# Kernel tuning notes

Hardware: AMD Instinct MI355X
Metric: run time of the kernel (lower is better)

Reference implementation:

```python
import jax, jax.numpy as jnp
import numpy as np
from functools import partial

B, T, N, D_IN = 64, 12, 1024, 1
H = 64            # rnn_units
E_DIM = 16        # embed_dim
K = 2             # cheb_k
HOR, OUT = 12, 1  # horizon, output_dim
KC2 = min(12, H)  # end_conv2 kernel width


def setup_inputs() -> dict:
    key = jax.random.key(0)
    ks = jax.random.split(key, 20)
    s = 0.1
    d = {}
    d["source"] = jax.random.normal(ks[0], (B, T, N, D_IN), dtype=jnp.float32)
    d["node_emb"] = jax.random.normal(ks[1], (N, E_DIM), dtype=jnp.float32)
    # per-encoder AGCRN cell hypernetwork pools (single layer: dim_in = D_IN)
    ci = D_IN + H  # concat(x, state) channel dim
    d["e1_gate_W"] = s * jax.random.normal(ks[2], (E_DIM, K, ci, 2 * H), dtype=jnp.float32)
    d["e1_gate_b"] = s * jax.random.normal(ks[3], (E_DIM, 2 * H), dtype=jnp.float32)
    d["e1_up_W"]   = s * jax.random.normal(ks[4], (E_DIM, K, ci, H), dtype=jnp.float32)
    d["e1_up_b"]   = s * jax.random.normal(ks[5], (E_DIM, H), dtype=jnp.float32)
    d["e2_gate_W"] = s * jax.random.normal(ks[6], (E_DIM, K, ci, 2 * H), dtype=jnp.float32)
    d["e2_gate_b"] = s * jax.random.normal(ks[7], (E_DIM, 2 * H), dtype=jnp.float32)
    d["e2_up_W"]   = s * jax.random.normal(ks[8], (E_DIM, K, ci, H), dtype=jnp.float32)
    d["e2_up_b"]   = s * jax.random.normal(ks[9], (E_DIM, H), dtype=jnp.float32)
    # end convs: Conv2d(1, HOR*OUT, kernel=(1, w)) -> weight [C_out, 1, 1, w]
    d["c1_W"] = s * jax.random.normal(ks[10], (HOR * OUT, 1, 1, H), dtype=jnp.float32)
    d["c1_b"] = s * jax.random.normal(ks[11], (HOR * OUT,), dtype=jnp.float32)
    d["c2_W"] = s * jax.random.normal(ks[12], (HOR * OUT, 1, 1, KC2), dtype=jnp.float32)
    d["c2_b"] = s * jax.random.normal(ks[13], (HOR * OUT,), dtype=jnp.float32)
    d["c3_W"] = s * jax.random.normal(ks[14], (HOR * OUT, 1, 1, H), dtype=jnp.float32)
    d["c3_b"] = s * jax.random.normal(ks[15], (HOR * OUT,), dtype=jnp.float32)
    return d


def _supports(E):
    # softmax(relu(E E^T), axis=1); cheb stack [I, A, 2A@T_{k-1}-T_{k-2}, ...]
    A = jax.nn.softmax(jax.nn.relu(E @ E.T), axis=1)
    sup = [jnp.eye(E.shape[0], dtype=E.dtype), A]
    for _ in range(2, K):
        sup.append(2.0 * A @ sup[-1] - sup[-2])
    return jnp.stack(sup[:K])  # [K, N, N]


def _encoder(x, E, supports, gate_W, gate_b, up_W, up_b):
    # x: [B, T, N, D_IN]; returns last hidden state [B, N, H]
    # hoist node-wise hypernetwork weights (independent of t)
    Wg = jnp.einsum('nd,dkio->nkio', E, gate_W)   # [N,K,ci,2H]
    bg = E @ gate_b                                # [N,2H]
    Wu = jnp.einsum('nd,dkio->nkio', E, up_W)      # [N,K,ci,H]
    bu = E @ up_b                                  # [N,H]

    def agc(z, W, b):
        # z: [B, N, C] -> [B, N, O]
        zg = jnp.einsum('knm,bmc->bnkc', supports, z)
        return jnp.einsum('bnkc,nkco->bno', zg, W) + b

    def step(h, xt):
        xs = jnp.concatenate([xt, h], axis=-1)                 # [B,N,ci]
        zr = jax.nn.sigmoid(agc(xs, Wg, bg))                   # [B,N,2H]
        z, r = zr[..., :H], zr[..., H:]
        cand = jnp.concatenate([xt, z * h], axis=-1)
        hc = jnp.tanh(agc(cand, Wu, bu))
        h_new = r * h + (1.0 - r) * hc
        return h_new, None

    h0 = jnp.zeros((x.shape[0], x.shape[2], H), dtype=x.dtype)
    h_last, _ = jax.lax.scan(step, h0, jnp.transpose(x, (1, 0, 2, 3)))
    return h_last


def reference(source, node_emb, e1_gate_W, e1_gate_b, e1_up_W, e1_up_b,
              e2_gate_W, e2_gate_b, e2_up_W, e2_up_b,
              c1_W, c1_b, c2_W, c2_b, c3_W, c3_b):
    supports = _supports(node_emb)
    # encoder 1 -> last state [B,N,H]
    h1 = _encoder(source, node_emb, supports, e1_gate_W, e1_gate_b, e1_up_W, e1_up_b)
    # end_conv1: Conv2d(1, HOR, (1,H)) on [B,1,N,H] -> [B,HOR,N,1]
    out1 = jnp.einsum('bnh,ch->bcn', h1, c1_W[:, 0, 0, :]) + c1_b[None, :, None]
    out1 = out1[..., None]                                     # [B,HOR,N,1]
    # end_conv2 on out1.permute(0,3,2,1) = [B,1,N,HOR]: contract channel axis
    src1 = jnp.einsum('bjn,cj->bcn', out1[..., 0], c2_W[:, 0, 0, :]) + c2_b[None, :, None]
    src1 = src1[..., None]                                     # [B,HOR,N,1] == [B,T,N,1]
    source2 = source - src1
    h2 = _encoder(source2, node_emb, supports, e2_gate_W, e2_gate_b, e2_up_W, e2_up_b)
    out2 = jnp.einsum('bnh,ch->bcn', h2, c3_W[:, 0, 0, :]) + c3_b[None, :, None]
    out2 = out2[..., None]
    return out1 + out2
```

## Files before the change

kernel.cpp:

```cpp
#include <hip/hip_runtime.h>

#define N_NODES 1024
#define T_STEPS 12
#define JW2     4224
#define NELEM   (N_NODES*JW2)

__device__ __forceinline__ float4 f4fma(float4 acc, float4 a, float s) {
    acc.x = fmaf(a.x, s, acc.x); acc.y = fmaf(a.y, s, acc.y);
    acc.z = fmaf(a.z, s, acc.z); acc.w = fmaf(a.w, s, acc.w);
    return acc;
}
__device__ __forceinline__ float4 sig4(float4 v, float b) {
    float4 r;
    r.x = 1.f/(1.f+expf(-(v.x+b))); r.y = 1.f/(1.f+expf(-(v.y+b)));
    r.z = 1.f/(1.f+expf(-(v.z+b))); r.w = 1.f/(1.f+expf(-(v.w+b)));
    return r;
}
__device__ __forceinline__ float4 tanh4(float4 v, float b) {
    float4 r;
    r.x = tanhf(v.x+b); r.y = tanhf(v.y+b);
    r.z = tanhf(v.z+b); r.w = tanhf(v.w+b);
    return r;
}

__global__ __launch_bounds__(256) void k_supports(const float* __restrict__ E,
                                                  float* __restrict__ A) {
    int n = blockIdx.x;
    int tid = threadIdx.x;
    __shared__ float en[16];
    __shared__ float red[256];
    if (tid < 16) en[tid] = E[n*16 + tid];
    __syncthreads();
    float s[4];
    float mx = -1e30f;
#pragma unroll
    for (int i = 0; i < 4; i++) {
        int m = tid + i*256;
        float acc = 0.f;
#pragma unroll
        for (int d = 0; d < 16; d++) acc += en[d]*E[m*16 + d];
        acc = fmaxf(acc, 0.f);
        s[i] = acc;
        mx = fmaxf(mx, acc);
    }
    red[tid] = mx; __syncthreads();
    for (int st = 128; st > 0; st >>= 1) {
        if (tid < st) red[tid] = fmaxf(red[tid], red[tid+st]);
        __syncthreads();
    }
    mx = red[0]; __syncthreads();
    float sum = 0.f;
#pragma unroll
    for (int i = 0; i < 4; i++) { s[i] = expf(s[i]-mx); sum += s[i]; }
    red[tid] = sum; __syncthreads();
    for (int st = 128; st > 0; st >>= 1) {
        if (tid < st) red[tid] += red[tid+st];
        __syncthreads();
    }
    float inv = 1.f / red[0];
#pragma unroll
    for (int i = 0; i < 4; i++) A[(size_t)n*1024 + tid + i*256] = s[i]*inv;
}

__global__ __launch_bounds__(256) void k_mix(const float* __restrict__ E,
                                             const float* __restrict__ Win,
                                             float* __restrict__ Wout, int SZ) {
    int idx = blockIdx.x*256 + threadIdx.x;
    if (idx >= SZ) return;
    float w[16];
#pragma unroll
    for (int d = 0; d < 16; d++) w[d] = Win[(size_t)d*SZ + idx];
    int n0 = blockIdx.y * 32;
    for (int n = n0; n < n0+32; n++) {
        float acc = 0.f;
#pragma unroll
        for (int d = 0; d < 16; d++) acc += E[n*16 + d]*w[d];
        Wout[(size_t)n*SZ + idx] = acc;
    }
}

__global__ __launch_bounds__(256) void k_init_xs(const float* __restrict__ src,
                                                 float* __restrict__ XS) {
    int i = blockIdx.x*256 + threadIdx.x;
    int col = i % JW2;
    int n   = i / JW2;
    float v = 0.f;
    if (col < 64) v = src[((size_t)col*T_STEPS)*N_NODES + n];
    XS[i] = v;
}

__global__ __launch_bounds__(256) void k_gemm(const float* __restrict__ A,
                                              const float* __restrict__ X,
                                              float* __restrict__ C) {
    __shared__ float As[32][68];
    __shared__ float Xs[32][68];
    int g = blockIdx.x;
    int xcd  = g & 7;
    int rank = g >> 3;
    int bx = rank >> 1;
    int by = xcd*2 + (rank & 1);
    int n0 = by * 64;
    int j0 = bx * 64;

    int tid = threadIdx.x;
    int tx = tid & 15, ty = tid >> 4;
    int arow = tid & 63, aseg = tid >> 6;
    int xk = tid >> 4, xcol = (tid & 15) * 4;

    float4 acc[4];
#pragma unroll
    for (int i = 0; i < 4; i++) acc[i] = make_float4(0.f,0.f,0.f,0.f);

    for (int kc = 0; kc < 1024; kc += 32) {
        float4 av0 = *(const float4*)&A[(size_t)(n0+arow)*1024 + kc + aseg*8];
        float4 av1 = *(const float4*)&A[(size_t)(n0+arow)*1024 + kc + aseg*8 + 4];
        float4 xv0 = *(const float4*)&X[(size_t)(kc + xk)*JW2 + j0 + xcol];
        float4 xv1 = *(const float4*)&X[(size_t)(kc + xk + 16)*JW2 + j0 + xcol];
        __syncthreads();
        As[aseg*8+0][arow] = av0.x; As[aseg*8+1][arow] = av0.y;
        As[aseg*8+2][arow] = av0.z; As[aseg*8+3][arow] = av0.w;
        As[aseg*8+4][arow] = av1.x; As[aseg*8+5][arow] = av1.y;
        As[aseg*8+6][arow] = av1.z; As[aseg*8+7][arow] = av1.w;
        *(float4*)&Xs[xk][xcol]      = xv0;
        *(float4*)&Xs[xk + 16][xcol] = xv1;
        __syncthreads();
#pragma unroll
        for (int kk = 0; kk < 32; kk++) {
            float4 a = *(float4*)&As[kk][ty*4];
            float4 b = *(float4*)&Xs[kk][tx*4];
            acc[0] = f4fma(acc[0], b, a.x);
            acc[1] = f4fma(acc[1], b, a.y);
            acc[2] = f4fma(acc[2], b, a.z);
            acc[3] = f4fma(acc[3], b, a.w);
        }
    }
#pragma unroll
    for (int i = 0; i < 4; i++)
        *(float4*)&C[(size_t)(n0 + ty*4 + i)*JW2 + j0 + tx*4] = acc[i];
}

__global__ __launch_bounds__(256) void k_gate(const float* __restrict__ XS,
                                              const float* __restrict__ ZG,
                                              const float* __restrict__ WG,
                                              const float* __restrict__ BG,
                                              float* __restrict__ CAND,
                                              float* __restrict__ Rb) {
    int n = blockIdx.x, tid = threadIdx.x;
    __shared__ float Zl[130*64];
    __shared__ float Wl[32*128];
    {
        const float4* xs4 = (const float4*)(XS + (size_t)n*JW2);
        const float4* z4  = (const float4*)(ZG + (size_t)n*JW2);
        float4* zl4 = (float4*)Zl;
        for (int i = tid; i < 1040; i += 256) zl4[i] = xs4[i];
        for (int i = tid; i < 1040; i += 256) zl4[1040 + i] = z4[i];
    }
    const float4* wg4 = (const float4*)(WG + (size_t)n*16640);
    float4 wreg0 = wg4[tid];
    float4 wreg1 = wg4[tid + 256];
    float4 wreg2 = wg4[tid + 512];
    float4 wreg3 = wg4[tid + 768];
    float wtail = 0.f;

    int jt = tid & 15, bt = tid >> 4;
    int j0 = jt*4, b0 = bt*4;
    float4 accz[4], accr[4];
#pragma unroll
    for (int i = 0; i < 4; i++) { accz[i] = make_float4(0,0,0,0); accr[i] = make_float4(0,0,0,0); }

    for (int c = 0; c < 5; c++) {
        int kc0 = c*32;
        int cnt = (c == 4) ? 2 : 32;
        __syncthreads();
        if (c < 4) {
            float4* wl4 = (float4*)Wl;
            wl4[tid]       = wreg0;
            wl4[tid + 256] = wreg1;
            wl4[tid + 512] = wreg2;
            wl4[tid + 768] = wreg3;
            if (c < 3) {
                wreg0 = wg4[(c+1)*1024 + tid];
                wreg1 = wg4[(c+1)*1024 + tid + 256];
                wreg2 = wg4[(c+1)*1024 + tid + 512];
                wreg3 = wg4[(c+1)*1024 + tid + 768];
            } else {
                wtail = WG[(size_t)n*16640 + 16384 + tid];
            }
        } else {
            Wl[tid] = wtail;
        }
        __syncthreads();
        for (int kk = 0; kk < cnt; kk++) {
            float4 a4 = *(float4*)&Zl[(kc0+kk)*64 + b0];
            float4 wz = *(float4*)&Wl[kk*128 + j0];
            float4 wr = *(float4*)&Wl[kk*128 + 64 + j0];
            float wza[4] = {wz.x,wz.y,wz.z,wz.w};
            float wra[4] = {wr.x,wr.y,wr.z,wr.w};
#pragma unroll
            for (int i = 0; i < 4; i++) {
                accz[i] = f4fma(accz[i], a4, wza[i]);
                accr[i] = f4fma(accr[i], a4, wra[i]);
            }
        }
    }
    const float* bg = BG + n*128;
#pragma unroll
    for (int i = 0; i < 4; i++) {
        int j = j0 + i;
        float4 z = sig4(accz[i], bg[j]);
        float4 r = sig4(accr[i], bg[64+j]);
        float4 h = *(const float4*)&XS[(size_t)n*JW2 + (1+j)*64 + b0];
        float4 zh; zh.x = z.x*h.x; zh.y = z.y*h.y; zh.z = z.z*h.z; zh.w = z.w*h.w;
        *(float4*)&CAND[(size_t)n*JW2 + (1+j)*64 + b0] = zh;
        *(float4*)&Rb[(size_t)n*4096 + j*64 + b0] = r;
    }
    if (tid < 16)
        ((float4*)(CAND + (size_t)n*JW2))[tid] = ((float4*)Zl)[tid];
}

__global__ __launch_bounds__(256) void k_up(const float* __restrict__ CAND,
                                            const float* __restrict__ CG,
                                            const float* __restrict__ WU,
                                            const float* __restrict__ BU,
                                            const float* __restrict__ Rb,
                                            float* __restrict__ XS,
                                            const float* __restrict__ src,
                                            int tnext, int hasNext) {
    int n = blockIdx.x, tid = threadIdx.x;
    __shared__ float Zl[130*64];
    __shared__ float Wl[32*64];
    {
        const float4* c4 = (const float4*)(CAND + (size_t)n*JW2);
        const float4* g4 = (const float4*)(CG + (size_t)n*JW2);
        float4* zl4 = (float4*)Zl;
        for (int i = tid; i < 1040; i += 256) zl4[i] = c4[i];
        for (int i = tid; i < 1040; i += 256) zl4[1040 + i] = g4[i];
    }
    const float4* wu4 = (const float4*)(WU + (size_t)n*8320);
    float4 wreg0 = wu4[tid];
    float4 wreg1 = wu4[tid + 256];
    float wtail = 0.f;

    int jt = tid & 15, bt = tid >> 4;
    int j0 = jt*4, b0 = bt*4;
    float4 acc[4];
#pragma unroll
    for (int i = 0; i < 4; i++) acc[i] = make_float4(0,0,0,0);

    for (int c = 0; c < 5; c++) {
        int kc0 = c*32;
        int cnt = (c == 4) ? 2 : 32;
        __syncthreads();
        if (c < 4) {
            float4* wl4 = (float4*)Wl;
            wl4[tid]       = wreg0;
            wl4[tid + 256] = wreg1;
            if (c < 3) {
                wreg0 = wu4[(c+1)*512 + tid];
                wreg1 = wu4[(c+1)*512 + tid + 256];
            } else if (tid < 128) {
                wtail = WU[(size_t)n*8320 + 8192 + tid];
            }
        } else {
            if (tid < 128) Wl[tid] = wtail;
        }
        __syncthreads();
        for (int kk = 0; kk < cnt; kk++) {
            float4 a4 = *(float4*)&Zl[(kc0+kk)*64 + b0];
            float4 w4 = *(float4*)&Wl[kk*64 + j0];
            float wa[4] = {w4.x,w4.y,w4.z,w4.w};
#pragma unroll
            for (int i = 0; i < 4; i++) acc[i] = f4fma(acc[i], a4, wa[i]);
        }
    }
    const float* bu = BU + n*64;
#pragma unroll
    for (int i = 0; i < 4; i++) {
        int j = j0 + i;
        float4 hc = tanh4(acc[i], bu[j]);
        float4 r  = *(const float4*)&Rb[(size_t)n*4096 + j*64 + b0];
        size_t xi = (size_t)n*JW2 + (1+j)*64 + b0;
        float4 hold = *(const float4*)&XS[xi];
        float4 hn;
        hn.x = r.x*hold.x + (1.f-r.x)*hc.x;
        hn.y = r.y*hold.y + (1.f-r.y)*hc.y;
        hn.z = r.z*hold.z + (1.f-r.z)*hc.z;
        hn.w = r.w*hold.w + (1.f-r.w)*hc.w;
        *(float4*)&XS[xi] = hn;
    }
    __syncthreads();
    if (hasNext && tid < 64)
        XS[(size_t)n*JW2 + tid] = src[((size_t)tid*T_STEPS + tnext)*N_NODES + n];
}

__global__ __launch_bounds__(256) void k_head1(const float* __restrict__ XS,
                                               const float* __restrict__ c1W,
                                               const float* __restrict__ c1b,
                                               const float* __restrict__ c2W,
                                               const float* __restrict__ c2b,
                                               const float* __restrict__ src,
                                               float* __restrict__ OUT1,
                                               float* __restrict__ SRC2) {
    int n = blockIdx.x, tid = threadIdx.x;
    __shared__ float Hl[64][65];
    __shared__ float w1[12][64];
    __shared__ float o1[64][13];
    for (int i = tid; i < 4096; i += 256) {
        int j = i >> 6, b = i & 63;
        Hl[b][j] = XS[(size_t)n*JW2 + 64 + i];
    }
    for (int i = tid; i < 768; i += 256) w1[i >> 6][i & 63] = c1W[i];
    __syncthreads();
    int b = tid & 63, cg = tid >> 6;
#pragma unroll
    for (int cc = 0; cc < 3; cc++) {
        int c = cg*3 + cc;
        float accv = c1b[c];
        for (int j = 0; j < 64; j++) accv += Hl[b][j]*w1[c][j];
        o1[b][c] = accv;
    }
    __syncthreads();
#pragma unroll
    for (int cc = 0; cc < 3; cc++) {
        int c = cg*3 + cc;
        float s1 = c2b[c];
#pragma unroll
        for (int j = 0; j < 12; j++) s1 += o1[b][j]*c2W[c*12 + j];
        size_t idx = ((size_t)b*12 + c)*1024 + n;
        OUT1[idx] = o1[b][c];
        SRC2[idx] = src[idx] - s1;
    }
}

__global__ __launch_bounds__(256) void k_head2(const float* __restrict__ XS,
                                               const float* __restrict__ c3W,
                                               const float* __restrict__ c3b,
                                               const float* __restrict__ OUT1,
                                               float* __restrict__ out) {
    int n = blockIdx.x, tid = threadIdx.x;
    __shared__ float Hl[64][65];
    __shared__ float w3[12][64];
    for (int i = tid; i < 4096; i += 256) {
        int j = i >> 6, b = i & 63;
        Hl[b][j] = XS[(size_t)n*JW2 + 64 + i];
    }
    for (int i = tid; i < 768; i += 256) w3[i >> 6][i & 63] = c3W[i];
    __syncthreads();
    int b = tid & 63, cg = tid >> 6;
#pragma unroll
    for (int cc = 0; cc < 3; cc++) {
        int c = cg*3 + cc;
        float accv = c3b[c];
        for (int j = 0; j < 64; j++) accv += Hl[b][j]*w3[c][j];
        size_t idx = ((size_t)b*12 + c)*1024 + n;
        out[idx] = OUT1[idx] + accv;
    }
}

extern "C" void kernel_launch(void* const* d_in, const int* in_sizes, int n_in,
                              void* d_out, int out_size, void* d_ws, size_t ws_size,
                              hipStream_t stream) {
    const float* src  = (const float*)d_in[0];
    const float* E    = (const float*)d_in[1];
    const float* e1gW = (const float*)d_in[2];
    const float* e1gb = (const float*)d_in[3];
    const float* e1uW = (const float*)d_in[4];
    const float* e1ub = (const float*)d_in[5];
    const float* e2gW = (const float*)d_in[6];
    const float* e2gb = (const float*)d_in[7];
    const float* e2uW = (const float*)d_in[8];
    const float* e2ub = (const float*)d_in[9];
    const float* c1W  = (const float*)d_in[10];
    const float* c1b  = (const float*)d_in[11];
    const float* c2W  = (const float*)d_in[12];
    const float* c2b  = (const float*)d_in[13];
    const float* c3W  = (const float*)d_in[14];
    const float* c3b  = (const float*)d_in[15];

    float* ws = (float*)d_ws;
    float* A    = ws;
    float* WG   = A    + 1048576;
    float* WU   = WG   + 17039360;
    float* BG   = WU   + 8519680;
    float* BU   = BG   + 131072;
    float* XS   = BU   + 65536;
    float* ZG   = XS   + NELEM;
    float* CAND = ZG   + NELEM;
    float* Rb   = CAND + NELEM;
    float* OUT1 = Rb   + 4194304;
    float* SRC2 = OUT1 + 786432;

    k_supports<<<N_NODES, 256, 0, stream>>>(E, A);

    auto run_encoder = [&](const float* s, const float* gW, const float* gb,
                           const float* uW, const float* ub) {
        k_mix<<<dim3(65, 32), 256, 0, stream>>>(E, gW, WG, 16640);
        k_mix<<<dim3(33, 32), 256, 0, stream>>>(E, uW, WU, 8320);
        k_mix<<<dim3(1, 32),  256, 0, stream>>>(E, gb, BG, 128);
        k_mix<<<dim3(1, 32),  256, 0, stream>>>(E, ub, BU, 64);
        k_init_xs<<<NELEM/256, 256, 0, stream>>>(s, XS);
        for (int t = 0; t < T_STEPS; t++) {
            k_gemm<<<1056, 256, 0, stream>>>(A, XS, ZG);
            k_gate<<<N_NODES, 256, 0, stream>>>(XS, ZG, WG, BG, CAND, Rb);
            k_gemm<<<1056, 256, 0, stream>>>(A, CAND, ZG);
            k_up<<<N_NODES, 256, 0, stream>>>(CAND, ZG, WU, BU, Rb, XS, s,
                                              t + 1, (t + 1 < T_STEPS) ? 1 : 0);
        }
    };

    run_encoder(src, e1gW, e1gb, e1uW, e1ub);
    k_head1<<<N_NODES, 256, 0, stream>>>(XS, c1W, c1b, c2W, c2b, src, OUT1, SRC2);
    run_encoder(SRC2, e2gW, e2gb, e2uW, e2ub);
    k_head2<<<N_NODES, 256, 0, stream>>>(XS, c3W, c3b, OUT1, (float*)d_out);
}
```

Measured before the change: 8.576 ms.

## Enlarge GEMM register tile to 8x8 with register prefetch and swizzled LDS

The support-matrix GEMM now uses 128-thread blocks, each computing a 64x128 output tile with an 8x8 register tile per thread instead of 4x4. The next K-chunk of A and X is loaded into registers while the current chunk is computed, which overlaps global latency with math. The X tile in shared memory uses an XOR column swizzle to reduce bank conflicts on the wider reads. In exchange, registers per thread rise and there are half as many blocks, which may lower occupancy.

```diff
diff --git a/kernel.cpp b/kernel.cpp
--- a/kernel.cpp
+++ b/kernel.cpp
@@ -89,54 +89,88 @@
     XS[i] = v;
 }
 
-__global__ __launch_bounds__(256) void k_gemm(const float* __restrict__ A,
-                                              const float* __restrict__ X,
-                                              float* __restrict__ C) {
+__device__ __forceinline__ int xs_phys(int g) { return g ^ ((g >> 3) & 1); }
+
+__global__ __launch_bounds__(128, 2) void k_gemm(const float* __restrict__ A,
+                                                 const float* __restrict__ X,
+                                                 float* __restrict__ C) {
     __shared__ float As[32][68];
-    __shared__ float Xs[32][68];
+    __shared__ float Xs[32][132];
     int g = blockIdx.x;
     int xcd  = g & 7;
     int rank = g >> 3;
     int bx = rank >> 1;
     int by = xcd*2 + (rank & 1);
     int n0 = by * 64;
-    int j0 = bx * 64;
+    int j0 = bx * 128;
 
     int tid = threadIdx.x;
     int tx = tid & 15, ty = tid >> 4;
+    int p0 = xs_phys(2*tx), p1 = xs_phys(2*tx + 1);
     int arow = tid & 63, aseg = tid >> 6;
-    int xk = tid >> 4, xcol = (tid & 15) * 4;
-
-    float4 acc[4];
-#pragma unroll
-    for (int i = 0; i < 4; i++) acc[i] = make_float4(0.f,0.f,0.f,0.f);
+    int xk = tid >> 4;
+
+    float4 pa[4];
+    float4 px[8];
+
+    const float* Abase = A + (size_t)(n0 + arow)*1024 + aseg*16;
+    const float* Xbase = X + (size_t)xk*JW2 + j0 + tx*8;
+
+#pragma unroll
+    for (int s = 0; s < 4; s++) pa[s] = *(const float4*)(Abase + s*4);
+#pragma unroll
+    for (int q = 0; q < 4; q++) {
+        px[2*q]   = *(const float4*)(Xbase + (size_t)(8*q)*JW2);
+        px[2*q+1] = *(const float4*)(Xbase + (size_t)(8*q)*JW2 + 4);
+    }
+
+    float4 acc[8][2];
+#pragma unroll
+    for (int i = 0; i < 8; i++) { acc[i][0] = make_float4(0,0,0,0); acc[i][1] = make_float4(0,0,0,0); }
 
     for (int kc = 0; kc < 1024; kc += 32) {
-        float4 av0 = *(const float4*)&A[(size_t)(n0+arow)*1024 + kc + aseg*8];
-        float4 av1 = *(const float4*)&A[(size_t)(n0+arow)*1024 + kc + aseg*8 + 4];
-        float4 xv0 = *(const float4*)&X[(size_t)(kc + xk)*JW2 + j0 + xcol];
-        float4 xv1 = *(const float4*)&X[(size_t)(kc + xk + 16)*JW2 + j0 + xcol];
-        __syncthreads();
-        As[aseg*8+0][arow] = av0.x; As[aseg*8+1][arow] = av0.y;
-        As[aseg*8+2][arow] = av0.z; As[aseg*8+3][arow] = av0.w;
-        As[aseg*8+4][arow] = av1.x; As[aseg*8+5][arow] = av1.y;
-        As[aseg*8+6][arow] = av1.z; As[aseg*8+7][arow] = av1.w;
-        *(float4*)&Xs[xk][xcol]      = xv0;
-        *(float4*)&Xs[xk + 16][xcol] = xv1;
-        __syncthreads();
+        __syncthreads();
+#pragma unroll
+        for (int s = 0; s < 4; s++) {
+            float va[4] = {pa[s].x, pa[s].y, pa[s].z, pa[s].w};
+#pragma unroll
+            for (int e = 0; e < 4; e++) As[aseg*16 + s*4 + e][arow] = va[e];
+        }
+#pragma unroll
+        for (int q = 0; q < 4; q++) {
+            *(float4*)&Xs[xk + 8*q][p0*4] = px[2*q];
+            *(float4*)&Xs[xk + 8*q][p1*4] = px[2*q+1];
+        }
+        __syncthreads();
+        if (kc + 32 < 1024) {
+#pragma unroll
+            for (int s = 0; s < 4; s++) pa[s] = *(const float4*)(Abase + kc + 32 + s*4);
+#pragma unroll
+            for (int q = 0; q < 4; q++) {
+                px[2*q]   = *(const float4*)(Xbase + (size_t)(kc + 32 + 8*q)*JW2);
+                px[2*q+1] = *(const float4*)(Xbase + (size_t)(kc + 32 + 8*q)*JW2 + 4);
+            }
+        }
 #pragma unroll
         for (int kk = 0; kk < 32; kk++) {
-            float4 a = *(float4*)&As[kk][ty*4];
-            float4 b = *(float4*)&Xs[kk][tx*4];
-            acc[0] = f4fma(acc[0], b, a.x);
-            acc[1] = f4fma(acc[1], b, a.y);
-            acc[2] = f4fma(acc[2], b, a.z);
-            acc[3] = f4fma(acc[3], b, a.w);
-        }
-    }
-#pragma unroll
-    for (int i = 0; i < 4; i++)
-        *(float4*)&C[(size_t)(n0 + ty*4 + i)*JW2 + j0 + tx*4] = acc[i];
+            float4 a0 = *(float4*)&As[kk][ty*8];
+            float4 a1 = *(float4*)&As[kk][ty*8 + 4];
+            float4 b0 = *(float4*)&Xs[kk][p0*4];
+            float4 b1 = *(float4*)&Xs[kk][p1*4];
+            float ar[8] = {a0.x,a0.y,a0.z,a0.w,a1.x,a1.y,a1.z,a1.w};
+#pragma unroll
+            for (int i = 0; i < 8; i++) {
+                acc[i][0] = f4fma(acc[i][0], b0, ar[i]);
+                acc[i][1] = f4fma(acc[i][1], b1, ar[i]);
+            }
+        }
+    }
+#pragma unroll
+    for (int i = 0; i < 8; i++) {
+        size_t row = (size_t)(n0 + ty*8 + i);
+        *(float4*)&C[row*JW2 + j0 + tx*8]     = acc[i][0];
+        *(float4*)&C[row*JW2 + j0 + tx*8 + 4] = acc[i][1];
+    }
 }
 
 __global__ __launch_bounds__(256) void k_gate(const float* __restrict__ XS,
@@ -400,9 +434,9 @@
         k_mix<<<dim3(1, 32),  256, 0, stream>>>(E, ub, BU, 64);
         k_init_xs<<<NELEM/256, 256, 0, stream>>>(s, XS);
         for (int t = 0; t < T_STEPS; t++) {
-            k_gemm<<<1056, 256, 0, stream>>>(A, XS, ZG);
+            k_gemm<<<528, 128, 0, stream>>>(A, XS, ZG);
             k_gate<<<N_NODES, 256, 0, stream>>>(XS, ZG, WG, BG, CAND, Rb);
-            k_gemm<<<1056, 256, 0, stream>>>(A, CAND, ZG);
+            k_gemm<<<528, 128, 0, stream>>>(A, CAND, ZG);
             k_up<<<N_NODES, 256, 0, stream>>>(CAND, ZG, WU, BU, Rb, XS, s,
                                               t + 1, (t + 1 < T_STEPS) ? 1 : 0);
         }
```

Result: slower. 12.03 ms (+40.3%).

## Enlarge GEMM tile to 128x128 with register prefetch of next K chunk

Applied to the files above, without the earlier changes.

The support-matrix GEMM moves from 64x64 tiles with 4x4 outputs per thread to 128x128 tiles with 8x8 outputs per thread and a 16-deep K chunk. The next chunk's global loads are issued into registers before the compute loop, so load latency overlaps the FMAs. This raises arithmetic intensity and cuts global and LDS traffic per FLOP. The cost is fewer blocks (264 instead of 1056), which may underfill the MI355X's CUs, and more registers per thread. The XCD-aware block swizzle is also dropped.

```diff
diff --git a/kernel.cpp b/kernel.cpp
--- a/kernel.cpp
+++ b/kernel.cpp
@@ -92,51 +92,73 @@
 __global__ __launch_bounds__(256) void k_gemm(const float* __restrict__ A,
                                               const float* __restrict__ X,
                                               float* __restrict__ C) {
-    __shared__ float As[32][68];
-    __shared__ float Xs[32][68];
-    int g = blockIdx.x;
-    int xcd  = g & 7;
-    int rank = g >> 3;
-    int bx = rank >> 1;
-    int by = xcd*2 + (rank & 1);
-    int n0 = by * 64;
-    int j0 = bx * 64;
-
+    __shared__ float As[16][132];
+    __shared__ float Xs[16][132];
     int tid = threadIdx.x;
     int tx = tid & 15, ty = tid >> 4;
-    int arow = tid & 63, aseg = tid >> 6;
-    int xk = tid >> 4, xcol = (tid & 15) * 4;
-
-    float4 acc[4];
-#pragma unroll
-    for (int i = 0; i < 4; i++) acc[i] = make_float4(0.f,0.f,0.f,0.f);
-
-    for (int kc = 0; kc < 1024; kc += 32) {
-        float4 av0 = *(const float4*)&A[(size_t)(n0+arow)*1024 + kc + aseg*8];
-        float4 av1 = *(const float4*)&A[(size_t)(n0+arow)*1024 + kc + aseg*8 + 4];
-        float4 xv0 = *(const float4*)&X[(size_t)(kc + xk)*JW2 + j0 + xcol];
-        float4 xv1 = *(const float4*)&X[(size_t)(kc + xk + 16)*JW2 + j0 + xcol];
-        __syncthreads();
-        As[aseg*8+0][arow] = av0.x; As[aseg*8+1][arow] = av0.y;
-        As[aseg*8+2][arow] = av0.z; As[aseg*8+3][arow] = av0.w;
-        As[aseg*8+4][arow] = av1.x; As[aseg*8+5][arow] = av1.y;
-        As[aseg*8+6][arow] = av1.z; As[aseg*8+7][arow] = av1.w;
-        *(float4*)&Xs[xk][xcol]      = xv0;
-        *(float4*)&Xs[xk + 16][xcol] = xv1;
-        __syncthreads();
-#pragma unroll
-        for (int kk = 0; kk < 32; kk++) {
-            float4 a = *(float4*)&As[kk][ty*4];
-            float4 b = *(float4*)&Xs[kk][tx*4];
-            acc[0] = f4fma(acc[0], b, a.x);
-            acc[1] = f4fma(acc[1], b, a.y);
-            acc[2] = f4fma(acc[2], b, a.z);
-            acc[3] = f4fma(acc[3], b, a.w);
-        }
-    }
-#pragma unroll
-    for (int i = 0; i < 4; i++)
-        *(float4*)&C[(size_t)(n0 + ty*4 + i)*JW2 + j0 + tx*4] = acc[i];
+    int tx4 = tx*4, ty4 = ty*4;
+    int n0 = blockIdx.y * 128;
+    int j0 = blockIdx.x * 128;
+    int arow = tid >> 1, ach = (tid & 1) * 8;
+    int xkk = tid >> 4, xjj = (tid & 15) * 8;
+
+    const float* Abase = A + (size_t)(n0 + arow)*1024 + ach;
+    const float* Xbase = X + (size_t)xkk*JW2 + j0 + xjj;
+
+    float4 av0 = *(const float4*)(Abase);
+    float4 av1 = *(const float4*)(Abase + 4);
+    float4 xv0 = *(const float4*)(Xbase);
+    float4 xv1 = *(const float4*)(Xbase + 4);
+
+    float4 acc[2][2][4];
+#pragma unroll
+    for (int a = 0; a < 2; a++)
+#pragma unroll
+        for (int b = 0; b < 2; b++)
+#pragma unroll
+            for (int r = 0; r < 4; r++) acc[a][b][r] = make_float4(0.f,0.f,0.f,0.f);
+
+    for (int kc = 0; kc < 1024; kc += 16) {
+        __syncthreads();
+        As[ach+0][arow] = av0.x; As[ach+1][arow] = av0.y;
+        As[ach+2][arow] = av0.z; As[ach+3][arow] = av0.w;
+        As[ach+4][arow] = av1.x; As[ach+5][arow] = av1.y;
+        As[ach+6][arow] = av1.z; As[ach+7][arow] = av1.w;
+        *(float4*)&Xs[xkk][xjj]   = xv0;
+        *(float4*)&Xs[xkk][xjj+4] = xv1;
+        __syncthreads();
+        if (kc + 16 < 1024) {
+            av0 = *(const float4*)(Abase + kc + 16);
+            av1 = *(const float4*)(Abase + kc + 16 + 4);
+            xv0 = *(const float4*)(Xbase + (size_t)(kc + 16)*JW2);
+            xv1 = *(const float4*)(Xbase + (size_t)(kc + 16)*JW2 + 4);
+        }
+#pragma unroll
+        for (int kk = 0; kk < 16; kk++) {
+            float4 a0 = *(float4*)&As[kk][ty4];
+            float4 a1 = *(float4*)&As[kk][64+ty4];
+            float4 b0 = *(float4*)&Xs[kk][tx4];
+            float4 b1 = *(float4*)&Xs[kk][64+tx4];
+            float aa0[4] = {a0.x,a0.y,a0.z,a0.w};
+            float aa1[4] = {a1.x,a1.y,a1.z,a1.w};
+#pragma unroll
+            for (int r = 0; r < 4; r++) {
+                acc[0][0][r] = f4fma(acc[0][0][r], b0, aa0[r]);
+                acc[0][1][r] = f4fma(acc[0][1][r], b1, aa0[r]);
+                acc[1][0][r] = f4fma(acc[1][0][r], b0, aa1[r]);
+                acc[1][1][r] = f4fma(acc[1][1][r], b1, aa1[r]);
+            }
+        }
+    }
+#pragma unroll
+    for (int a = 0; a < 2; a++)
+#pragma unroll
+        for (int r = 0; r < 4; r++) {
+            int row = n0 + a*64 + ty4 + r;
+#pragma unroll
+            for (int b = 0; b < 2; b++)
+                *(float4*)&C[(size_t)row*JW2 + j0 + b*64 + tx4] = acc[a][b][r];
+        }
 }
 
 __global__ __launch_bounds__(256) void k_gate(const float* __restrict__ XS,
@@ -400,9 +422,9 @@
         k_mix<<<dim3(1, 32),  256, 0, stream>>>(E, ub, BU, 64);
         k_init_xs<<<NELEM/256, 256, 0, stream>>>(s, XS);
         for (int t = 0; t < T_STEPS; t++) {
-            k_gemm<<<1056, 256, 0, stream>>>(A, XS, ZG);
+            k_gemm<<<dim3(33, 8), 256, 0, stream>>>(A, XS, ZG);
             k_gate<<<N_NODES, 256, 0, stream>>>(XS, ZG, WG, BG, CAND, Rb);
-            k_gemm<<<1056, 256, 0, stream>>>(A, CAND, ZG);
+            k_gemm<<<dim3(33, 8), 256, 0, stream>>>(A, CAND, ZG);
             k_up<<<N_NODES, 256, 0, stream>>>(CAND, ZG, WU, BU, Rb, XS, s,
                                               t + 1, (t + 1 < T_STEPS) ? 1 : 0);
         }
```

After: 10.18 ms. 1.19x slower.
